# Optimization experiments

Measured on AMD Instinct MI355X. Metric: run time of the kernel, lower is better.

Reference implementation:

```python
import jax, jax.numpy as jnp
import numpy as np

C, S, Q, P, D = 5, 5, 75, 196, 384  # ways, shots, queries, patches, feat dim
K = 30  # topk in enhancePrototypes / featureWalk


def _bn(x, g, b, eps=1e-5):
    # BatchNorm1d in training mode: batch statistics (biased var)
    m = x.mean(axis=0)
    v = x.var(axis=0)
    return g * (x - m) * jax.lax.rsqrt(v + eps) + b


def _mlp(x, W1, b1, g1, be1, al, W2, b2, g2, be2):
    # fc1 -> bn1 -> PReLU -> (dropout=identity, eval) -> fc2 -> bn2
    h = _bn(x @ W1 + b1, g1, be1)
    h = jnp.where(h >= 0, h, al * h)
    h = h @ W2 + b2
    return _bn(h, g2, be2)


def _enhance_prototypes(cls_tok, patch, k=K, a=1.0):
    # cls_tok: (C,S,D), patch: (C,S,P,D)
    dist = jnp.linalg.norm(cls_tok[:, :, None, :] - patch, axis=3)  # (C,S,P)
    d0 = dist[:, 0, :]                       # (C,P) -- source uses [0] row
    other = d0.sum(axis=0)[None, :] - d0     # sum over other classes, shot 0
    sim = dist / (other[:, None, :] + 1e-6)  # (C,S,P)
    _, idx = jax.lax.top_k(sim, k)           # (C,S,k)
    sel = jnp.take_along_axis(patch, idx[..., None], axis=2)  # (C,S,k,D)
    return cls_tok * 2.0 + a * sel.mean(axis=2)


def _feature_walk(prototypes, q_patch, cls_tok, k=K, a=1.0):
    # prototypes: (C,D), q_patch: (Q,P,D), cls_tok: (Q,D)
    dot = jnp.einsum('cd,qpd->cqp', prototypes, q_patch)
    n_p = jnp.linalg.norm(prototypes, axis=1)      # (C,)
    n_q = jnp.linalg.norm(q_patch, axis=2)         # (Q,P)
    cos = dot / jnp.maximum(n_p[:, None, None] * n_q[None], 1e-8)
    w = jax.nn.softmax(cos, axis=2)                # (C,Q,P)
    vals, idx = jax.lax.top_k(w, k)                # (C,Q,k)
    gathered = q_patch[jnp.arange(Q)[None, :, None], idx]  # (C,Q,k,D)
    wsum = jnp.einsum('cqk,cqkd->cqd', vals, gathered)
    return cls_tok[None] * 2.0 + a * wsum          # (C,Q,D)


def setup_inputs() -> dict:
    key = jax.random.key(0)
    ks = jax.random.split(key, 12)
    r = lambda i, shape, s=1.0: jax.random.normal(ks[i], shape, dtype=jnp.float32) * s
    inp = {
        'support_set_vectors': r(0, (C * S, 1, D)),
        'query_set_vectors': r(1, (Q, 1, D)),
        'dalle_emb_support': r(2, (C * S, 1, D)),
        'emb_patch_support': r(3, (C * S, P, D)),
        'emb_patch_query': r(4, (Q, P, D)),
        'dalle_patch_embedding': r(5, (C * S, P, D)),
    }
    i = 6
    for pre in ('da', 'pa'):
        inp[pre + '_W1'] = r(i, (D, D), 0.05)
        inp[pre + '_b1'] = jnp.zeros((D,), jnp.float32)
        inp[pre + '_g1'] = jnp.ones((D,), jnp.float32)
        inp[pre + '_be1'] = jnp.zeros((D,), jnp.float32)
        inp[pre + '_al'] = jnp.float32(0.25)  # PReLU default init
        inp[pre + '_W2'] = r(i + 1, (D, D), 0.05)
        inp[pre + '_b2'] = jnp.zeros((D,), jnp.float32)
        inp[pre + '_g2'] = jnp.ones((D,), jnp.float32)
        inp[pre + '_be2'] = jnp.zeros((D,), jnp.float32)
        i += 2
    return inp


def reference(support_set_vectors, query_set_vectors, dalle_emb_support,
              emb_patch_support, emb_patch_query, dalle_patch_embedding,
              da_W1, da_b1, da_g1, da_be1, da_al, da_W2, da_b2, da_g2, da_be2,
              pa_W1, pa_b1, pa_g1, pa_be1, pa_al, pa_W2, pa_b2, pa_g2, pa_be2):
    da = (da_W1, da_b1, da_g1, da_be1, da_al, da_W2, da_b2, da_g2, da_be2)
    pa = (pa_W1, pa_b1, pa_g1, pa_be1, pa_al, pa_W2, pa_b2, pa_g2, pa_be2)

    sup = support_set_vectors.reshape(C, S, D)
    qcls = query_set_vectors.reshape(Q, D)

    dalle_sup = _mlp(dalle_emb_support.reshape(-1, D), *da).reshape(C, S, D)
    dalle_patch = _mlp(dalle_patch_embedding.reshape(-1, D), *da).reshape(-1, P, D)

    eps_ = emb_patch_support + _mlp(emb_patch_support.reshape(-1, D), *pa).reshape(-1, P, D)
    epq = emb_patch_query + _mlp(emb_patch_query.reshape(-1, D), *pa).reshape(-1, P, D)
    dalle_patch = dalle_patch + _mlp(dalle_patch.reshape(-1, D), *pa).reshape(-1, P, D)

    ep = jnp.concatenate([
        _enhance_prototypes(sup, eps_.reshape(C, S, P, D)),
        _enhance_prototypes(dalle_sup, dalle_patch.reshape(C, S, P, D)),
    ], axis=1).mean(axis=1)  # (C,D)

    cls_with_weighted_sums = _feature_walk(ep, epq, qcls)  # (C,Q,D)
    return ep, cls_with_weighted_sums
```

## Files before the change

### kernel.cpp

```cpp
#include <hip/hip_runtime.h>


#define CC 5
#define SS 5
#define QQ 75
#define PP 196
#define DD 384
#define KK 30
#define QP (QQ * PP)

typedef short bf16x8 __attribute__((ext_vector_type(8)));
typedef float f32x4  __attribute__((ext_vector_type(4)));
typedef unsigned short us16x4 __attribute__((ext_vector_type(4)));
typedef unsigned short us16x8 __attribute__((ext_vector_type(8)));
typedef unsigned short u16;

struct SegDesc { int b0, b1; float invM; };

__device__ __forceinline__ u16 f2bf(float f) {
    unsigned u = __float_as_uint(f);
    unsigned r = (u + 0x7fffu + ((u >> 16) & 1u)) >> 16;
    return (u16)r;
}
__device__ __forceinline__ float bf2f(u16 h) {
    return __uint_as_float((unsigned)h << 16);
}

__device__ __forceinline__ void lds_load16(const u16* g, u16* s) {
    __builtin_amdgcn_global_load_lds(
        (const __attribute__((address_space(1))) unsigned int*)g,
        (__attribute__((address_space(3))) unsigned int*)s, 16, 0, 0);
}

__device__ __forceinline__ bool grid_decode(int mb, int& mblk, int& nb) {
    int bid = blockIdx.x;
    int g = bid / 24, t24 = bid - g * 24;
    nb = t24 >> 3;
    mblk = g * 8 + (t24 & 7);
    return mblk < mb;
}

__device__ __forceinline__ void do_mfma64(const u16* Asb, const u16* Bsb,
                                          int wr, int wc, int l, f32x4 (&acc)[2][4]) {
#pragma unroll
    for (int ks = 0; ks < 2; ++ks) {
        bf16x8 af[2], bg[4];
#pragma unroll
        for (int i = 0; i < 2; ++i) {
            int rm = wr * 32 + i * 16 + (l & 15);
            af[i] = *(const bf16x8*)&Asb[rm * 64 + (((ks << 2) + (l >> 4)) ^ (rm & 7)) * 8];
        }
#pragma unroll
        for (int j = 0; j < 4; ++j) {
            int rn = wc * 64 + j * 16 + (l & 15);
            bg[j] = *(const bf16x8*)&Bsb[rn * 64 + (((ks << 2) + (l >> 4)) ^ (rn & 7)) * 8];
        }
#pragma unroll
        for (int i = 0; i < 2; ++i)
#pragma unroll
            for (int j = 0; j < 4; ++j)
                acc[i][j] = __builtin_amdgcn_mfma_f32_16x16x32_bf16(af[i], bg[j], acc[i][j], 0, 0, 0);
    }
}

__global__ void prep_w4(const float* __restrict__ W0, const float* __restrict__ W1,
                        const float* __restrict__ W2, const float* __restrict__ W3,
                        u16* __restrict__ Wt) {
    int idx = blockIdx.x * 256 + threadIdx.x;
    int m = idx / (DD * DD);
    int rem = idx - m * (DD * DD);
    int n = rem / DD, k = rem - n * DD;
    const float* W = (m == 0) ? W0 : (m == 1) ? W1 : (m == 2) ? W2 : W3;
    Wt[idx] = f2bf(W[k * DD + n]);
}

__global__ __launch_bounds__(256) void gemmF(const float* __restrict__ s0p,
                                             const float* __restrict__ s1p,
                                             const float* __restrict__ s2p,
                                             int rb0, int rb1, int M0, int M1, int M2,
                                             const u16* __restrict__ Bt,
                                             u16* __restrict__ H,
                                             float* __restrict__ partial, int mb) {
    __shared__ __align__(16) u16 As[2][4096];
    __shared__ __align__(16) u16 Bs[2][8192];
    __shared__ float sred[2][2][64][2];
    int mblk, nb;
    if (!grid_decode(mb, mblk, nb)) return;
    const int m0 = mblk * 64, n0 = nb * 128;
    const int tid = threadIdx.x;
    const int w = tid >> 6, l = tid & 63;
    const int wr = w >> 1, wc = w & 1;
    const int lr8 = l >> 3, kpB = l & 7;
    const int arow = tid >> 2, kp0 = (tid & 3) * 2;
    const int aslot0 = kp0 ^ (arow & 7);

    const int seg = (m0 >= rb0) + (m0 >= rb1);
    const float* src = seg == 0 ? s0p : seg == 1 ? s1p : s2p;
    const int segbase = seg == 0 ? 0 : seg == 1 ? rb0 : rb1;
    const int Mseg = seg == 0 ? M0 : seg == 1 ? M1 : M2;
    const int rloc = m0 - segbase + arow;

    f32x4 acc[2][4];
#pragma unroll
    for (int i = 0; i < 2; ++i)
#pragma unroll
        for (int j = 0; j < 4; ++j) acc[i][j] = f32x4{0.f, 0.f, 0.f, 0.f};

    f32x4 ra[4];
    auto issueA = [&](int kta) {
#pragma unroll
        for (int i = 0; i < 4; ++i) ra[i] = f32x4{0.f, 0.f, 0.f, 0.f};
        if (rloc < Mseg) {
            const f32x4* sp = (const f32x4*)(src + (size_t)rloc * DD + kta * 64 + kp0 * 8);
#pragma unroll
            for (int i = 0; i < 4; ++i) ra[i] = sp[i];
        }
    };
    auto stageB = [&](int kta, int b) {
#pragma unroll
        for (int i = 0; i < 4; ++i) {
            int row = i * 32 + w * 8 + lr8;
            lds_load16(Bt + (size_t)(n0 + row) * DD + kta * 64 + (kpB ^ (row & 7)) * 8,
                       &Bs[b][i * 2048 + w * 512]);
        }
    };
    auto writeA = [&](int b) {
        us16x8 o0, o1;
        o0[0] = f2bf(ra[0].x); o0[1] = f2bf(ra[0].y); o0[2] = f2bf(ra[0].z); o0[3] = f2bf(ra[0].w);
        o0[4] = f2bf(ra[1].x); o0[5] = f2bf(ra[1].y); o0[6] = f2bf(ra[1].z); o0[7] = f2bf(ra[1].w);
        o1[0] = f2bf(ra[2].x); o1[1] = f2bf(ra[2].y); o1[2] = f2bf(ra[2].z); o1[3] = f2bf(ra[2].w);
        o1[4] = f2bf(ra[3].x); o1[5] = f2bf(ra[3].y); o1[6] = f2bf(ra[3].z); o1[7] = f2bf(ra[3].w);
        *(us16x8*)&As[b][arow * 64 + aslot0 * 8] = o0;
        *(us16x8*)&As[b][arow * 64 + (aslot0 ^ 1) * 8] = o1;
    };

    issueA(0);
    stageB(0, 0);
    writeA(0);
    __syncthreads();
    int cur = 0;
    for (int kt = 0; kt < 5; ++kt) {
        int nxt = cur ^ 1;
        issueA(kt + 1);
        stageB(kt + 1, nxt);
        do_mfma64(&As[cur][0], &Bs[cur][0], wr, wc, l, acc);
        writeA(nxt);
        __syncthreads();
        cur = nxt;
    }
    do_mfma64(&As[cur][0], &Bs[cur][0], wr, wc, l, acc);

#pragma unroll
    for (int i = 0; i < 2; ++i) {
        int rw0 = m0 + wr * 32 + i * 16 + ((l >> 4) << 2);
#pragma unroll
        for (int j = 0; j < 4; ++j) {
            int col = n0 + wc * 64 + j * 16 + (l & 15);
#pragma unroll
            for (int r = 0; r < 4; ++r)
                H[(size_t)(rw0 + r) * DD + col] = f2bf(acc[i][j][r]);
        }
    }
    float ls[4], ls2[4];
#pragma unroll
    for (int j = 0; j < 4; ++j) { ls[j] = 0.f; ls2[j] = 0.f; }
#pragma unroll
    for (int i = 0; i < 2; ++i)
#pragma unroll
        for (int j = 0; j < 4; ++j)
#pragma unroll
            for (int r = 0; r < 4; ++r) {
                float v = acc[i][j][r];
                ls[j] += v; ls2[j] += v * v;
            }
#pragma unroll
    for (int j = 0; j < 4; ++j) {
        ls[j]  += __shfl_xor(ls[j], 16);  ls[j]  += __shfl_xor(ls[j], 32);
        ls2[j] += __shfl_xor(ls2[j], 16); ls2[j] += __shfl_xor(ls2[j], 32);
    }
    if ((l >> 4) == 0) {
#pragma unroll
        for (int j = 0; j < 4; ++j) {
            sred[wr][wc][j * 16 + (l & 15)][0] = ls[j];
            sred[wr][wc][j * 16 + (l & 15)][1] = ls2[j];
        }
    }
    __syncthreads();
    if (tid < 128) {
        int wcx = tid >> 6, c64 = tid & 63;
        float sa = sred[0][wcx][c64][0] + sred[1][wcx][c64][0];
        float sb = sred[0][wcx][c64][1] + sred[1][wcx][c64][1];
        size_t pi = ((size_t)mblk * DD + n0 + tid) * 2;
        partial[pi] = sa; partial[pi + 1] = sb;
    }
}

__global__ __launch_bounds__(256) void gemmA(const u16* __restrict__ Hs,
                                             int rb0, int rb1, int M0, int M1, int M2,
                                             const u16* __restrict__ Bt,
                                             const float* __restrict__ alp,
                                             const float* __restrict__ mstats,
                                             u16* __restrict__ H2,
                                             float* __restrict__ partial, int mb) {
    __shared__ __align__(16) u16 As[2][4096];
    __shared__ __align__(16) u16 Bs[2][8192];
    __shared__ float sred[2][2][64][2];
    __shared__ __align__(16) float msL[768];
    int mblk, nb;
    if (!grid_decode(mb, mblk, nb)) return;
    const int m0 = mblk * 64, n0 = nb * 128;
    const int tid = threadIdx.x;
    const int w = tid >> 6, l = tid & 63;
    const int wr = w >> 1, wc = w & 1;
    const int lr8 = l >> 3, kpB = l & 7;
    const int arow = tid >> 2, kp0 = (tid & 3) * 2;
    const int aslot0 = kp0 ^ (arow & 7);

    const int seg = (m0 >= rb0) + (m0 >= rb1);
    const int segbase = seg == 0 ? 0 : seg == 1 ? rb0 : rb1;
    const int Mseg = seg == 0 ? M0 : seg == 1 ? M1 : M2;
    const int rloc = m0 - segbase + arow;
    const float al = *alp;

    if (tid < 192) ((f32x4*)msL)[tid] = ((const f32x4*)(mstats + seg * 768))[tid];

    f32x4 acc[2][4];
#pragma unroll
    for (int i = 0; i < 2; ++i)
#pragma unroll
        for (int j = 0; j < 4; ++j) acc[i][j] = f32x4{0.f, 0.f, 0.f, 0.f};

    us16x8 rh[2];
    auto issueA = [&](int kta) {
        rh[0] = us16x8{0, 0, 0, 0, 0, 0, 0, 0};
        rh[1] = us16x8{0, 0, 0, 0, 0, 0, 0, 0};
        if (rloc < Mseg) {
            const us16x8* sp = (const us16x8*)(Hs + (size_t)(m0 + arow) * DD + kta * 64 + kp0 * 8);
            rh[0] = sp[0]; rh[1] = sp[1];
        }
    };
    auto stageB = [&](int kta, int b) {
#pragma unroll
        for (int i = 0; i < 4; ++i) {
            int row = i * 32 + w * 8 + lr8;
            lds_load16(Bt + (size_t)(n0 + row) * DD + kta * 64 + (kpB ^ (row & 7)) * 8,
                       &Bs[b][i * 2048 + w * 512]);
        }
    };
    auto writeA = [&](int kta, int b) {
        int cb = kta * 64 + kp0 * 8;
        us16x8 o0 = {0, 0, 0, 0, 0, 0, 0, 0}, o1 = {0, 0, 0, 0, 0, 0, 0, 0};
        if (rloc < Mseg) {
            f32x4 sc0 = *(const f32x4*)&msL[cb];
            f32x4 sc1 = *(const f32x4*)&msL[cb + 4];
            f32x4 sc2 = *(const f32x4*)&msL[cb + 8];
            f32x4 sc3 = *(const f32x4*)&msL[cb + 12];
            f32x4 sh0 = *(const f32x4*)&msL[384 + cb];
            f32x4 sh1 = *(const f32x4*)&msL[384 + cb + 4];
            f32x4 sh2 = *(const f32x4*)&msL[384 + cb + 8];
            f32x4 sh3 = *(const f32x4*)&msL[384 + cb + 12];
            float v;
            v = bf2f(rh[0][0]) * sc0.x + sh0.x; v = v >= 0.f ? v : al * v; o0[0] = f2bf(v);
            v = bf2f(rh[0][1]) * sc0.y + sh0.y; v = v >= 0.f ? v : al * v; o0[1] = f2bf(v);
            v = bf2f(rh[0][2]) * sc0.z + sh0.z; v = v >= 0.f ? v : al * v; o0[2] = f2bf(v);
            v = bf2f(rh[0][3]) * sc0.w + sh0.w; v = v >= 0.f ? v : al * v; o0[3] = f2bf(v);
            v = bf2f(rh[0][4]) * sc1.x + sh1.x; v = v >= 0.f ? v : al * v; o0[4] = f2bf(v);
            v = bf2f(rh[0][5]) * sc1.y + sh1.y; v = v >= 0.f ? v : al * v; o0[5] = f2bf(v);
            v = bf2f(rh[0][6]) * sc1.z + sh1.z; v = v >= 0.f ? v : al * v; o0[6] = f2bf(v);
            v = bf2f(rh[0][7]) * sc1.w + sh1.w; v = v >= 0.f ? v : al * v; o0[7] = f2bf(v);
            v = bf2f(rh[1][0]) * sc2.x + sh2.x; v = v >= 0.f ? v : al * v; o1[0] = f2bf(v);
            v = bf2f(rh[1][1]) * sc2.y + sh2.y; v = v >= 0.f ? v : al * v; o1[1] = f2bf(v);
            v = bf2f(rh[1][2]) * sc2.z + sh2.z; v = v >= 0.f ? v : al * v; o1[2] = f2bf(v);
            v = bf2f(rh[1][3]) * sc2.w + sh2.w; v = v >= 0.f ? v : al * v; o1[3] = f2bf(v);
            v = bf2f(rh[1][4]) * sc3.x + sh3.x; v = v >= 0.f ? v : al * v; o1[4] = f2bf(v);
            v = bf2f(rh[1][5]) * sc3.y + sh3.y; v = v >= 0.f ? v : al * v; o1[5] = f2bf(v);
            v = bf2f(rh[1][6]) * sc3.z + sh3.z; v = v >= 0.f ? v : al * v; o1[6] = f2bf(v);
            v = bf2f(rh[1][7]) * sc3.w + sh3.w; v = v >= 0.f ? v : al * v; o1[7] = f2bf(v);
        }
        *(us16x8*)&As[b][arow * 64 + aslot0 * 8] = o0;
        *(us16x8*)&As[b][arow * 64 + (aslot0 ^ 1) * 8] = o1;
    };

    issueA(0);
    stageB(0, 0);
    __syncthreads();
    writeA(0, 0);
    __syncthreads();
    int cur = 0;
    for (int kt = 0; kt < 5; ++kt) {
        int nxt = cur ^ 1;
        issueA(kt + 1);
        stageB(kt + 1, nxt);
        do_mfma64(&As[cur][0], &Bs[cur][0], wr, wc, l, acc);
        writeA(kt + 1, nxt);
        __syncthreads();
        cur = nxt;
    }
    do_mfma64(&As[cur][0], &Bs[cur][0], wr, wc, l, acc);

#pragma unroll
    for (int i = 0; i < 2; ++i) {
        int rw0 = m0 + wr * 32 + i * 16 + ((l >> 4) << 2);
#pragma unroll
        for (int j = 0; j < 4; ++j) {
            int col = n0 + wc * 64 + j * 16 + (l & 15);
#pragma unroll
            for (int r = 0; r < 4; ++r)
                H2[(size_t)(rw0 + r) * DD + col] = f2bf(acc[i][j][r]);
        }
    }
    float ls[4], ls2[4];
#pragma unroll
    for (int j = 0; j < 4; ++j) { ls[j] = 0.f; ls2[j] = 0.f; }
#pragma unroll
    for (int i = 0; i < 2; ++i)
#pragma unroll
        for (int j = 0; j < 4; ++j)
#pragma unroll
            for (int r = 0; r < 4; ++r) {
                float v = acc[i][j][r];
                ls[j] += v; ls2[j] += v * v;
            }
#pragma unroll
    for (int j = 0; j < 4; ++j) {
        ls[j]  += __shfl_xor(ls[j], 16);  ls[j]  += __shfl_xor(ls[j], 32);
        ls2[j] += __shfl_xor(ls2[j], 16); ls2[j] += __shfl_xor(ls2[j], 32);
    }
    if ((l >> 4) == 0) {
#pragma unroll
        for (int j = 0; j < 4; ++j) {
            sred[wr][wc][j * 16 + (l & 15)][0] = ls[j];
            sred[wr][wc][j * 16 + (l & 15)][1] = ls2[j];
        }
    }
    __syncthreads();
    if (tid < 128) {
        int wcx = tid >> 6, c64 = tid & 63;
        float sa = sred[0][wcx][c64][0] + sred[1][wcx][c64][0];
        float sb = sred[0][wcx][c64][1] + sred[1][wcx][c64][1];
        size_t pi = ((size_t)mblk * DD + n0 + tid) * 2;
        partial[pi] = sa; partial[pi + 1] = sb;
    }
}

__global__ void colfin(const float* __restrict__ partial, SegDesc s0, SegDesc s1,
                       SegDesc s2, const float* __restrict__ g,
                       const float* __restrict__ be, float* __restrict__ mstats) {
    int seg = blockIdx.x / 12, cg = blockIdx.x - seg * 12;
    SegDesc sd = (seg == 0) ? s0 : (seg == 1) ? s1 : s2;
    int tid = threadIdx.x;
    int col = cg * 32 + (tid & 31);
    int part = tid >> 5;
    float sa = 0.f, sb = 0.f;
    for (int b = sd.b0 + part; b < sd.b1; b += 8) {
        size_t pi = ((size_t)b * DD + col) * 2;
        sa += partial[pi]; sb += partial[pi + 1];
    }
    __shared__ float red[256][2];
    red[tid][0] = sa; red[tid][1] = sb;
    __syncthreads();
    for (int st = 128; st >= 32; st >>= 1) {
        if (tid < st) { red[tid][0] += red[tid + st][0]; red[tid][1] += red[tid + st][1]; }
        __syncthreads();
    }
    if (tid < 32) {
        float m = red[tid][0] * sd.invM;
        float var = fmaxf(red[tid][1] * sd.invM - m * m, 0.f);
        float iv = rsqrtf(var + 1e-5f);
        int c = cg * 32 + tid;
        float sc = iv * g[c];
        mstats[seg * 768 + c] = sc;
        mstats[seg * 768 + 384 + c] = be[c] - m * sc;
    }
}

__global__ void mlp_out_k(const u16* __restrict__ H, const float* __restrict__ mstats,
                          const float* __restrict__ res0, float* __restrict__ out0,
                          const float* __restrict__ res1, float* __restrict__ out1,
                          const float* __restrict__ res2, float* __restrict__ out2,
                          int rb0, int rb1, int M0, int M1, int M2) {
    int idx4 = blockIdx.x * 256 + threadIdx.x;
    int row = idx4 / 96, cq = idx4 - row * 96, col = cq * 4;
    int seg = (row >= rb0) + (row >= rb1);
    int vr = row - (seg == 1 ? rb0 : seg == 2 ? rb1 : 0);
    int M = seg == 0 ? M0 : seg == 1 ? M1 : M2;
    const float* res = seg == 0 ? res0 : seg == 1 ? res1 : res2;
    float* outf = seg == 0 ? out0 : seg == 1 ? out1 : out2;
    f32x4 v = {0.f, 0.f, 0.f, 0.f};
    if (vr < M) {
        us16x4 h = ((const us16x4*)H)[idx4];
        const float* ms = mstats + seg * 768;
        f32x4 sc = *(const f32x4*)(ms + col);
        f32x4 sh = *(const f32x4*)(ms + 384 + col);
        v.x = bf2f(h.x) * sc.x + sh.x;
        v.y = bf2f(h.y) * sc.y + sh.y;
        v.z = bf2f(h.z) * sc.z + sh.z;
        v.w = bf2f(h.w) * sc.w + sh.w;
        if (res) {
            f32x4 r = ((const f32x4*)res)[(size_t)vr * 96 + cq];
            v.x += r.x; v.y += r.y; v.z += r.z; v.w += r.w;
        }
    }
    ((f32x4*)outf)[(size_t)vr * 96 + cq] = v;
}

__global__ void dist_k(const float* __restrict__ epsP, const float* __restrict__ dpfP,
                       const float* __restrict__ supC, const float* __restrict__ dsupC,
                       float* __restrict__ dist) {
    int id = blockIdx.x;
    int b = id / (CC * SS * PP);
    int r = id - b * (CC * SS * PP);
    int cs = r / PP;
    const float* patch = b ? dpfP : epsP;
    const float* cls = b ? dsupC : supC;
    int l = threadIdx.x;
    const float* pr = patch + (size_t)r * DD;
    const float* cr = cls + (size_t)cs * DD;
    float s = 0.f;
    for (int d = l; d < DD; d += 64) { float df = cr[d] - pr[d]; s += df * df; }
#pragma unroll
    for (int off = 32; off > 0; off >>= 1) s += __shfl_xor(s, off);
    if (l == 0) dist[id] = sqrtf(s);
}

__global__ void enh_k(const float* __restrict__ dist, const float* __restrict__ epsP,
                      const float* __restrict__ dpfP, const float* __restrict__ supC,
                      const float* __restrict__ dsupC, float* __restrict__ enh) {
    int id = blockIdx.x;
    int b = id / 25, cs = id - b * 25, c = cs / SS;
    int t = threadIdx.x;
    __shared__ float sim[PP];
    __shared__ int sidx[KK];
    const float* db = dist + b * (CC * SS * PP);
    if (t < PP) {
        float osum = 0.f;
        for (int cc = 0; cc < CC; ++cc) osum += db[cc * SS * PP + t];
        float other = osum - db[c * SS * PP + t];
        sim[t] = db[cs * PP + t] / (other + 1e-6f);
    }
    __syncthreads();
    if (t < PP) {
        float mine = sim[t];
        int cnt = 0;
        for (int p = 0; p < PP; ++p) {
            float v = sim[p];
            cnt += (v > mine) || (v == mine && p < t);
        }
        if (cnt < KK) sidx[cnt] = t;
    }
    __syncthreads();
    const float* patch = b ? dpfP : epsP;
    const float* cls = b ? dsupC : supC;
    float sum = 0.f;
#pragma unroll
    for (int j = 0; j < KK; ++j) sum += patch[((size_t)cs * PP + sidx[j]) * DD + t];
    enh[(size_t)id * DD + t] = 2.f * cls[(size_t)cs * DD + t] + sum * (1.f / 30.f);
}

__global__ void ep_k(const float* __restrict__ enh, float* __restrict__ outEp,
                     float* __restrict__ npb) {
    int t = threadIdx.x;
    __shared__ float red[DD];
    for (int c = 0; c < CC; ++c) {
        float v = 0.f;
        for (int b = 0; b < 2; ++b)
            for (int s = 0; s < SS; ++s)
                v += enh[((b * 25) + (c * SS + s)) * DD + t];
        v *= 0.1f;
        outEp[c * DD + t] = v;
        red[t] = v * v;
        __syncthreads();
        if (t < 64) {
            float s = 0.f;
            for (int i = t; i < DD; i += 64) s += red[i];
#pragma unroll
            for (int off = 32; off > 0; off >>= 1) s += __shfl_xor(s, off);
            if (t == 0) npb[c] = sqrtf(s);
        }
        __syncthreads();
    }
}

__global__ void cos_k(const float* __restrict__ epq, const float* __restrict__ ep,
                      const float* __restrict__ npb, float* __restrict__ eB) {
    __shared__ __align__(16) float epl[CC * DD];
    __shared__ float npl[CC];
    int t = threadIdx.x;
    for (int i = t; i < CC * DD; i += 256) epl[i] = ep[i];
    if (t < CC) npl[t] = npb[t];
    __syncthreads();
    int wid = t >> 6, l = t & 63;
    int row = blockIdx.x * 4 + wid;
    const float4* rp = (const float4*)(epq + (size_t)row * DD);
    const float4* e4 = (const float4*)epl;
    float nq = 0.f, dot[CC];
#pragma unroll
    for (int c = 0; c < CC; ++c) dot[c] = 0.f;
    for (int c4 = l; c4 < DD / 4; c4 += 64) {
        float4 x = rp[c4];
        nq += x.x * x.x + x.y * x.y + x.z * x.z + x.w * x.w;
#pragma unroll
        for (int c = 0; c < CC; ++c) {
            float4 e = e4[c * (DD / 4) + c4];
            dot[c] += e.x * x.x + e.y * x.y + e.z * x.z + e.w * x.w;
        }
    }
#pragma unroll
    for (int off = 32; off > 0; off >>= 1) {
        nq += __shfl_xor(nq, off);
#pragma unroll
        for (int c = 0; c < CC; ++c) dot[c] += __shfl_xor(dot[c], off);
    }
    if (l == 0) {
        float sq = sqrtf(nq);
#pragma unroll
        for (int c = 0; c < CC; ++c)
            eB[c * QP + row] = expf(dot[c] / fmaxf(npl[c] * sq, 1e-8f) - 1.f);
    }
}

__global__ void walk2_k(const float* __restrict__ eB, const float* __restrict__ epq,
                        const float* __restrict__ qcls, float* __restrict__ outp) {
    int bid = blockIdx.x;
    int c = bid / QQ, q = bid - c * QQ;
    int t = threadIdx.x;
    __shared__ float wv[PP];
    __shared__ float red[256];
    __shared__ float sval[KK];
    __shared__ int sidx[KK];
    float e = 0.f;
    if (t < PP) { e = eB[c * QP + q * PP + t]; wv[t] = e; }
    red[t] = e;
    __syncthreads();
    for (int st = 128; st > 0; st >>= 1) { if (t < st) red[t] += red[t + st]; __syncthreads(); }
    float inv = 1.f / red[0];
    if (t < PP) {
        int cnt = 0;
        for (int p = 0; p < PP; ++p) {
            float v = wv[p];
            cnt += (v > e) || (v == e && p < t);
        }
        if (cnt < KK) { sval[cnt] = e * inv; sidx[cnt] = t; }
    }
    __syncthreads();
    const float* eb = epq + (size_t)q * PP * DD;
    for (int d = t; d < DD; d += 256) {
        float a = 0.f;
#pragma unroll
        for (int j = 0; j < KK; ++j) a += sval[j] * eb[(size_t)sidx[j] * DD + d];
        outp[(size_t)bid * DD + d] = 2.f * qcls[q * DD + d] + a;
    }
}

extern "C" void kernel_launch(void* const* d_in, const int* in_sizes, int n_in,
                              void* d_out, int out_size, void* d_ws, size_t ws_size,
                              hipStream_t stream) {
    const float* sup   = (const float*)d_in[0];
    const float* qcls  = (const float*)d_in[1];
    const float* dsupI = (const float*)d_in[2];
    const float* epsI  = (const float*)d_in[3];
    const float* epqI  = (const float*)d_in[4];
    const float* dpI   = (const float*)d_in[5];
    const float* daW1 = (const float*)d_in[6],  *daG1 = (const float*)d_in[8],
               * daBe1 = (const float*)d_in[9], *daAl = (const float*)d_in[10];
    const float* daW2 = (const float*)d_in[11], *daG2 = (const float*)d_in[13],
               * daBe2 = (const float*)d_in[14];
    const float* paW1 = (const float*)d_in[15], *paG1 = (const float*)d_in[17],
               * paBe1 = (const float*)d_in[18], *paAl = (const float*)d_in[19];
    const float* paW2 = (const float*)d_in[20], *paG2 = (const float*)d_in[22],
               * paBe2 = (const float*)d_in[23];

    char* ws = (char*)d_ws;
    size_t off = 0;
    auto alloc = [&](size_t b) -> void* {
        void* p = ws + off;
        off = (off + b + 255) & ~(size_t)255;
        return p;
    };
    const int MP_S = 128;
    const int M_P = 4900,  MP_P = 4992;
    const int M_Q = 14700, MP_Qa = 14848;
    const int ROWS_A  = MP_S + MP_P;
    const int ROWS_BC = MP_P + MP_Qa + MP_P;
    const int RB0 = MP_P, RB1 = MP_P + MP_Qa;

    u16*   wtAll = (u16*)alloc((size_t)4 * DD * DD * 2);
    u16*   wtDa1 = wtAll;
    u16*   wtDa2 = wtAll + DD * DD;
    u16*   wtPa1 = wtAll + 2 * DD * DD;
    u16*   wtPa2 = wtAll + 3 * DD * DD;
    u16*   hbuf  = (u16*)alloc((size_t)ROWS_BC * DD * 2);
    u16*   a2buf = (u16*)alloc((size_t)ROWS_BC * DD * 2);
    float* partial = (float*)alloc((size_t)(ROWS_BC / 64) * DD * 2 * 4);
    float* mstats  = (float*)alloc(3 * 768 * 4);
    float* dalleSup = (float*)alloc((size_t)MP_S * DD * 4);
    float* dp0   = (float*)alloc((size_t)MP_P * DD * 4);
    float* epsB  = (float*)alloc((size_t)MP_P * DD * 4);
    float* epqB  = (float*)alloc((size_t)MP_Qa * DD * 4);
    float* dpfB  = (float*)alloc((size_t)MP_P * DD * 4);
    float* distB = (float*)alloc((size_t)2 * CC * SS * PP * 4);
    float* enhB  = (float*)alloc((size_t)50 * DD * 4);
    float* npB   = (float*)alloc(64);
    float* eB    = (float*)alloc((size_t)CC * QP * 4);

    prep_w4<<<4 * 576, 256, 0, stream>>>(daW1, daW2, paW1, paW2, wtAll);

    {
        int mb = ROWS_A / 64;
        int nblk = ((mb + 7) / 8) * 24;
        SegDesc s0{0, 2, 1.f / 25.f}, s1{2, mb, 1.f / 4900.f}, sx{0, 0, 1.f};
        int g96 = (ROWS_A * 96) / 256;
        gemmF<<<nblk, 256, 0, stream>>>(dsupI, dpI, nullptr, MP_S, ROWS_A,
                                        25, M_P, 0, wtDa1, hbuf, partial, mb);
        colfin<<<24, 256, 0, stream>>>(partial, s0, s1, sx, daG1, daBe1, mstats);
        gemmA<<<nblk, 256, 0, stream>>>(hbuf, MP_S, ROWS_A, 25, M_P, 0,
                                        wtDa2, daAl, mstats, a2buf, partial, mb);
        colfin<<<24, 256, 0, stream>>>(partial, s0, s1, sx, daG2, daBe2, mstats);
        mlp_out_k<<<g96, 256, 0, stream>>>(a2buf, mstats,
                                           nullptr, dalleSup,
                                           nullptr, dp0,
                                           nullptr, nullptr,
                                           MP_S, ROWS_A, 25, M_P, 0);
    }

    {
        int mb = ROWS_BC / 64;
        int nblk = ((mb + 7) / 8) * 24;
        SegDesc s0{0, RB0 / 64, 1.f / 4900.f},
                s1{RB0 / 64, RB1 / 64, 1.f / 14700.f},
                s2{RB1 / 64, mb, 1.f / 4900.f};
        int g96 = (ROWS_BC * 96) / 256;
        gemmF<<<nblk, 256, 0, stream>>>(epsI, epqI, dp0, RB0, RB1,
                                        M_P, M_Q, M_P, wtPa1, hbuf, partial, mb);
        colfin<<<36, 256, 0, stream>>>(partial, s0, s1, s2, paG1, paBe1, mstats);
        gemmA<<<nblk, 256, 0, stream>>>(hbuf, RB0, RB1, M_P, M_Q, M_P,
                                        wtPa2, paAl, mstats, a2buf, partial, mb);
        colfin<<<36, 256, 0, stream>>>(partial, s0, s1, s2, paG2, paBe2, mstats);
        mlp_out_k<<<g96, 256, 0, stream>>>(a2buf, mstats,
                                           epsI, epsB,
                                           epqI, epqB,
                                           dp0, dpfB,
                                           RB0, RB1, M_P, M_Q, M_P);
    }

    dist_k<<<2 * CC * SS * PP, 64, 0, stream>>>(epsB, dpfB, sup, dalleSup, distB);
    enh_k<<<2 * CC * SS, 384, 0, stream>>>(distB, epsB, dpfB, sup, dalleSup, enhB);

    float* outEp = (float*)d_out;
    float* outW = (float*)d_out + CC * DD;
    ep_k<<<1, 384, 0, stream>>>(enhB, outEp, npB);

    cos_k<<<QP / 4, 256, 0, stream>>>(epqB, outEp, npB, eB);
    walk2_k<<<CC * QQ, 256, 0, stream>>>(eB, epqB, qcls, outW);
}
```

Measured before the change: 177.3 us.

## Fuse tail stages into one cooperative persistent kernel with grid syncs

Replaces the last colfin, mlp_out, dist, enhance, ep, cos and walk kernels with a single cooperative kernel of 375 blocks that runs each stage in turn, separated by grid.sync(). The aim is to remove the launch overhead and inter-kernel gaps of seven small launches. In exchange, the large elementwise and cosine stages now run on only 375 blocks using grid-stride loops, and each grid barrier has its own cost. Several stages also leave most blocks idle.

```diff
diff --git a/kernel.cpp b/kernel.cpp
--- a/kernel.cpp
+++ b/kernel.cpp
@@ -1,4 +1,7 @@
 #include <hip/hip_runtime.h>
+#include <hip/hip_cooperative_groups.h>
+
+namespace cg = cooperative_groups;
 
 
 #define CC 5
@@ -346,10 +349,10 @@
 __global__ void colfin(const float* __restrict__ partial, SegDesc s0, SegDesc s1,
                        SegDesc s2, const float* __restrict__ g,
                        const float* __restrict__ be, float* __restrict__ mstats) {
-    int seg = blockIdx.x / 12, cg = blockIdx.x - seg * 12;
+    int seg = blockIdx.x / 12, cg_ = blockIdx.x - seg * 12;
     SegDesc sd = (seg == 0) ? s0 : (seg == 1) ? s1 : s2;
     int tid = threadIdx.x;
-    int col = cg * 32 + (tid & 31);
+    int col = cg_ * 32 + (tid & 31);
     int part = tid >> 5;
     float sa = 0.f, sb = 0.f;
     for (int b = sd.b0 + part; b < sd.b1; b += 8) {
@@ -367,7 +370,7 @@
         float m = red[tid][0] * sd.invM;
         float var = fmaxf(red[tid][1] * sd.invM - m * m, 0.f);
         float iv = rsqrtf(var + 1e-5f);
-        int c = cg * 32 + tid;
+        int c = cg_ * 32 + tid;
         float sc = iv * g[c];
         mstats[seg * 768 + c] = sc;
         mstats[seg * 768 + 384 + c] = be[c] - m * sc;
@@ -404,151 +407,216 @@
     ((f32x4*)outf)[(size_t)vr * 96 + cq] = v;
 }
 
-__global__ void dist_k(const float* __restrict__ epsP, const float* __restrict__ dpfP,
-                       const float* __restrict__ supC, const float* __restrict__ dsupC,
-                       float* __restrict__ dist) {
-    int id = blockIdx.x;
-    int b = id / (CC * SS * PP);
-    int r = id - b * (CC * SS * PP);
-    int cs = r / PP;
-    const float* patch = b ? dpfP : epsP;
-    const float* cls = b ? dsupC : supC;
-    int l = threadIdx.x;
-    const float* pr = patch + (size_t)r * DD;
-    const float* cr = cls + (size_t)cs * DD;
-    float s = 0.f;
-    for (int d = l; d < DD; d += 64) { float df = cr[d] - pr[d]; s += df * df; }
-#pragma unroll
-    for (int off = 32; off > 0; off >>= 1) s += __shfl_xor(s, off);
-    if (l == 0) dist[id] = sqrtf(s);
-}
-
-__global__ void enh_k(const float* __restrict__ dist, const float* __restrict__ epsP,
-                      const float* __restrict__ dpfP, const float* __restrict__ supC,
-                      const float* __restrict__ dsupC, float* __restrict__ enh) {
-    int id = blockIdx.x;
-    int b = id / 25, cs = id - b * 25, c = cs / SS;
-    int t = threadIdx.x;
+struct TailArgs {
+    const float* partial; SegDesc s0, s1, s2;
+    const float* g2; const float* be2; float* mstats;
+    const u16* H2;
+    const float* res0; float* out0;
+    const float* res1; float* out1;
+    const float* res2; float* out2;
+    int rb0, rb1, M0, M1, M2;
+    const float* supC; const float* dsupC;
+    float* dist; float* enh;
+    float* outEp; float* npb;
+    const float* qcls; float* eB; float* outW;
+};
+
+__global__ __launch_bounds__(256) void tail_k(TailArgs a) {
+    cg::grid_group grid = cg::this_grid();
+    const int bid = blockIdx.x;
+    const int tid = threadIdx.x;
+    const int wid = tid >> 6, l = tid & 63;
+    __shared__ float red2[256][2];
+    __shared__ float red1[256];
     __shared__ float sim[PP];
-    __shared__ int sidx[KK];
-    const float* db = dist + b * (CC * SS * PP);
-    if (t < PP) {
-        float osum = 0.f;
-        for (int cc = 0; cc < CC; ++cc) osum += db[cc * SS * PP + t];
-        float other = osum - db[c * SS * PP + t];
-        sim[t] = db[cs * PP + t] / (other + 1e-6f);
-    }
-    __syncthreads();
-    if (t < PP) {
-        float mine = sim[t];
-        int cnt = 0;
-        for (int p = 0; p < PP; ++p) {
-            float v = sim[p];
-            cnt += (v > mine) || (v == mine && p < t);
-        }
-        if (cnt < KK) sidx[cnt] = t;
-    }
-    __syncthreads();
-    const float* patch = b ? dpfP : epsP;
-    const float* cls = b ? dsupC : supC;
-    float sum = 0.f;
-#pragma unroll
-    for (int j = 0; j < KK; ++j) sum += patch[((size_t)cs * PP + sidx[j]) * DD + t];
-    enh[(size_t)id * DD + t] = 2.f * cls[(size_t)cs * DD + t] + sum * (1.f / 30.f);
-}
-
-__global__ void ep_k(const float* __restrict__ enh, float* __restrict__ outEp,
-                     float* __restrict__ npb) {
-    int t = threadIdx.x;
-    __shared__ float red[DD];
-    for (int c = 0; c < CC; ++c) {
-        float v = 0.f;
-        for (int b = 0; b < 2; ++b)
-            for (int s = 0; s < SS; ++s)
-                v += enh[((b * 25) + (c * SS + s)) * DD + t];
-        v *= 0.1f;
-        outEp[c * DD + t] = v;
-        red[t] = v * v;
-        __syncthreads();
-        if (t < 64) {
-            float s = 0.f;
-            for (int i = t; i < DD; i += 64) s += red[i];
-#pragma unroll
-            for (int off = 32; off > 0; off >>= 1) s += __shfl_xor(s, off);
-            if (t == 0) npb[c] = sqrtf(s);
-        }
-        __syncthreads();
-    }
-}
-
-__global__ void cos_k(const float* __restrict__ epq, const float* __restrict__ ep,
-                      const float* __restrict__ npb, float* __restrict__ eB) {
+    __shared__ float wv[PP];
+    __shared__ float sval[KK];
+    __shared__ int   sidx[KK];
     __shared__ __align__(16) float epl[CC * DD];
     __shared__ float npl[CC];
-    int t = threadIdx.x;
-    for (int i = t; i < CC * DD; i += 256) epl[i] = ep[i];
-    if (t < CC) npl[t] = npb[t];
+
+    if (bid < 36) {
+        int seg = bid / 12, cgp = bid - seg * 12;
+        SegDesc sd = (seg == 0) ? a.s0 : (seg == 1) ? a.s1 : a.s2;
+        int col = cgp * 32 + (tid & 31);
+        int part = tid >> 5;
+        float sa = 0.f, sb = 0.f;
+        for (int b = sd.b0 + part; b < sd.b1; b += 8) {
+            size_t pi = ((size_t)b * DD + col) * 2;
+            sa += a.partial[pi]; sb += a.partial[pi + 1];
+        }
+        red2[tid][0] = sa; red2[tid][1] = sb;
+        __syncthreads();
+        for (int st = 128; st >= 32; st >>= 1) {
+            if (tid < st) { red2[tid][0] += red2[tid + st][0]; red2[tid][1] += red2[tid + st][1]; }
+            __syncthreads();
+        }
+        if (tid < 32) {
+            float m = red2[tid][0] * sd.invM;
+            float var = fmaxf(red2[tid][1] * sd.invM - m * m, 0.f);
+            float iv = rsqrtf(var + 1e-5f);
+            int c = cgp * 32 + tid;
+            float sc = iv * a.g2[c];
+            a.mstats[seg * 768 + c] = sc;
+            a.mstats[seg * 768 + 384 + c] = a.be2[c] - m * sc;
+        }
+    }
+    grid.sync();
+
+    for (int chunk = bid; chunk < 9312; chunk += 375) {
+        int idx4 = chunk * 256 + tid;
+        int row = idx4 / 96, cq = idx4 - row * 96, col = cq * 4;
+        int seg = (row >= a.rb0) + (row >= a.rb1);
+        int vr = row - (seg == 1 ? a.rb0 : seg == 2 ? a.rb1 : 0);
+        int M = seg == 0 ? a.M0 : seg == 1 ? a.M1 : a.M2;
+        const float* res = seg == 0 ? a.res0 : seg == 1 ? a.res1 : a.res2;
+        float* outf = seg == 0 ? a.out0 : seg == 1 ? a.out1 : a.out2;
+        f32x4 v = {0.f, 0.f, 0.f, 0.f};
+        if (vr < M) {
+            us16x4 h = ((const us16x4*)a.H2)[idx4];
+            const float* ms = a.mstats + seg * 768;
+            f32x4 sc = *(const f32x4*)(ms + col);
+            f32x4 sh = *(const f32x4*)(ms + 384 + col);
+            v.x = bf2f(h.x) * sc.x + sh.x;
+            v.y = bf2f(h.y) * sc.y + sh.y;
+            v.z = bf2f(h.z) * sc.z + sh.z;
+            v.w = bf2f(h.w) * sc.w + sh.w;
+            f32x4 r = ((const f32x4*)res)[(size_t)vr * 96 + cq];
+            v.x += r.x; v.y += r.y; v.z += r.z; v.w += r.w;
+        }
+        ((f32x4*)outf)[(size_t)vr * 96 + cq] = v;
+    }
+    grid.sync();
+
+    for (int id = bid * 4 + wid; id < 2 * CC * SS * PP; id += 1500) {
+        int b = id / (CC * SS * PP);
+        int r = id - b * (CC * SS * PP);
+        int cs = r / PP;
+        const float* patch = b ? a.out2 : a.out0;
+        const float* cls = b ? a.dsupC : a.supC;
+        const float* pr = patch + (size_t)r * DD;
+        const float* cr = cls + (size_t)cs * DD;
+        float s = 0.f;
+        for (int d = l; d < DD; d += 64) { float df = cr[d] - pr[d]; s += df * df; }
+#pragma unroll
+        for (int off = 32; off > 0; off >>= 1) s += __shfl_xor(s, off);
+        if (l == 0) a.dist[id] = sqrtf(s);
+    }
+    grid.sync();
+
+    if (bid < 50) {
+        int b = bid / 25, cs = bid - b * 25, c = cs / SS;
+        const float* db = a.dist + b * (CC * SS * PP);
+        if (tid < PP) {
+            float osum = 0.f;
+            for (int cc = 0; cc < CC; ++cc) osum += db[cc * SS * PP + tid];
+            float other = osum - db[c * SS * PP + tid];
+            sim[tid] = db[cs * PP + tid] / (other + 1e-6f);
+        }
+        __syncthreads();
+        if (tid < PP) {
+            float mine = sim[tid];
+            int cnt = 0;
+            for (int p = 0; p < PP; ++p) {
+                float v = sim[p];
+                cnt += (v > mine) || (v == mine && p < tid);
+            }
+            if (cnt < KK) sidx[cnt] = tid;
+        }
+        __syncthreads();
+        const float* patch = b ? a.out2 : a.out0;
+        const float* cls = b ? a.dsupC : a.supC;
+        for (int d = tid; d < DD; d += 256) {
+            float sum = 0.f;
+#pragma unroll
+            for (int j = 0; j < KK; ++j) sum += patch[((size_t)cs * PP + sidx[j]) * DD + d];
+            a.enh[(size_t)bid * DD + d] = 2.f * cls[(size_t)cs * DD + d] + sum * (1.f / 30.f);
+        }
+    }
+    grid.sync();
+
+    if (bid < CC) {
+        int c = bid;
+        float ss = 0.f;
+        for (int t = tid; t < DD; t += 256) {
+            float v = 0.f;
+            for (int b = 0; b < 2; ++b)
+                for (int s = 0; s < SS; ++s)
+                    v += a.enh[((b * 25) + (c * SS + s)) * DD + t];
+            v *= 0.1f;
+            a.outEp[c * DD + t] = v;
+            ss += v * v;
+        }
+        red1[tid] = ss;
+        __syncthreads();
+        for (int st = 128; st > 0; st >>= 1) {
+            if (tid < st) red1[tid] += red1[tid + st];
+            __syncthreads();
+        }
+        if (tid == 0) a.npb[c] = sqrtf(red1[0]);
+    }
+    grid.sync();
+
+    for (int i = tid; i < CC * DD; i += 256) epl[i] = a.outEp[i];
+    if (tid < CC) npl[tid] = a.npb[tid];
     __syncthreads();
-    int wid = t >> 6, l = t & 63;
-    int row = blockIdx.x * 4 + wid;
-    const float4* rp = (const float4*)(epq + (size_t)row * DD);
-    const float4* e4 = (const float4*)epl;
-    float nq = 0.f, dot[CC];
-#pragma unroll
-    for (int c = 0; c < CC; ++c) dot[c] = 0.f;
-    for (int c4 = l; c4 < DD / 4; c4 += 64) {
-        float4 x = rp[c4];
-        nq += x.x * x.x + x.y * x.y + x.z * x.z + x.w * x.w;
-#pragma unroll
-        for (int c = 0; c < CC; ++c) {
-            float4 e = e4[c * (DD / 4) + c4];
-            dot[c] += e.x * x.x + e.y * x.y + e.z * x.z + e.w * x.w;
-        }
-    }
-#pragma unroll
-    for (int off = 32; off > 0; off >>= 1) {
-        nq += __shfl_xor(nq, off);
-#pragma unroll
-        for (int c = 0; c < CC; ++c) dot[c] += __shfl_xor(dot[c], off);
-    }
-    if (l == 0) {
-        float sq = sqrtf(nq);
-#pragma unroll
-        for (int c = 0; c < CC; ++c)
-            eB[c * QP + row] = expf(dot[c] / fmaxf(npl[c] * sq, 1e-8f) - 1.f);
-    }
-}
-
-__global__ void walk2_k(const float* __restrict__ eB, const float* __restrict__ epq,
-                        const float* __restrict__ qcls, float* __restrict__ outp) {
-    int bid = blockIdx.x;
-    int c = bid / QQ, q = bid - c * QQ;
-    int t = threadIdx.x;
-    __shared__ float wv[PP];
-    __shared__ float red[256];
-    __shared__ float sval[KK];
-    __shared__ int sidx[KK];
-    float e = 0.f;
-    if (t < PP) { e = eB[c * QP + q * PP + t]; wv[t] = e; }
-    red[t] = e;
-    __syncthreads();
-    for (int st = 128; st > 0; st >>= 1) { if (t < st) red[t] += red[t + st]; __syncthreads(); }
-    float inv = 1.f / red[0];
-    if (t < PP) {
-        int cnt = 0;
-        for (int p = 0; p < PP; ++p) {
-            float v = wv[p];
-            cnt += (v > e) || (v == e && p < t);
-        }
-        if (cnt < KK) { sval[cnt] = e * inv; sidx[cnt] = t; }
-    }
-    __syncthreads();
-    const float* eb = epq + (size_t)q * PP * DD;
-    for (int d = t; d < DD; d += 256) {
-        float a = 0.f;
-#pragma unroll
-        for (int j = 0; j < KK; ++j) a += sval[j] * eb[(size_t)sidx[j] * DD + d];
-        outp[(size_t)bid * DD + d] = 2.f * qcls[q * DD + d] + a;
+    for (int row = bid * 4 + wid; row < QP; row += 1500) {
+        const float4* rp = (const float4*)(a.out1 + (size_t)row * DD);
+        const float4* e4 = (const float4*)epl;
+        float nq = 0.f, dot[CC];
+#pragma unroll
+        for (int c = 0; c < CC; ++c) dot[c] = 0.f;
+        for (int c4 = l; c4 < DD / 4; c4 += 64) {
+            float4 x = rp[c4];
+            nq += x.x * x.x + x.y * x.y + x.z * x.z + x.w * x.w;
+#pragma unroll
+            for (int c = 0; c < CC; ++c) {
+                float4 e = e4[c * (DD / 4) + c4];
+                dot[c] += e.x * x.x + e.y * x.y + e.z * x.z + e.w * x.w;
+            }
+        }
+#pragma unroll
+        for (int off = 32; off > 0; off >>= 1) {
+            nq += __shfl_xor(nq, off);
+#pragma unroll
+            for (int c = 0; c < CC; ++c) dot[c] += __shfl_xor(dot[c], off);
+        }
+        if (l == 0) {
+            float sq = sqrtf(nq);
+#pragma unroll
+            for (int c = 0; c < CC; ++c)
+                a.eB[c * QP + row] = expf(dot[c] / fmaxf(npl[c] * sq, 1e-8f) - 1.f);
+        }
+    }
+    grid.sync();
+
+    {
+        int c = bid / QQ, q = bid - c * QQ;
+        float e = 0.f;
+        if (tid < PP) { e = a.eB[c * QP + q * PP + tid]; wv[tid] = e; }
+        red1[tid] = e;
+        __syncthreads();
+        for (int st = 128; st > 0; st >>= 1) {
+            if (tid < st) red1[tid] += red1[tid + st];
+            __syncthreads();
+        }
+        float inv = 1.f / red1[0];
+        if (tid < PP) {
+            int cnt = 0;
+            for (int p = 0; p < PP; ++p) {
+                float v = wv[p];
+                cnt += (v > e) || (v == e && p < tid);
+            }
+            if (cnt < KK) { sval[cnt] = e * inv; sidx[cnt] = tid; }
+        }
+        __syncthreads();
+        const float* eb = a.out1 + (size_t)q * PP * DD;
+        for (int d = tid; d < DD; d += 256) {
+            float acc = 0.f;
+#pragma unroll
+            for (int j = 0; j < KK; ++j) acc += sval[j] * eb[(size_t)sidx[j] * DD + d];
+            a.outW[(size_t)bid * DD + d] = 2.f * a.qcls[q * DD + d] + acc;
+        }
     }
 }
 
@@ -629,27 +697,28 @@
         SegDesc s0{0, RB0 / 64, 1.f / 4900.f},
                 s1{RB0 / 64, RB1 / 64, 1.f / 14700.f},
                 s2{RB1 / 64, mb, 1.f / 4900.f};
-        int g96 = (ROWS_BC * 96) / 256;
         gemmF<<<nblk, 256, 0, stream>>>(epsI, epqI, dp0, RB0, RB1,
                                         M_P, M_Q, M_P, wtPa1, hbuf, partial, mb);
         colfin<<<36, 256, 0, stream>>>(partial, s0, s1, s2, paG1, paBe1, mstats);
         gemmA<<<nblk, 256, 0, stream>>>(hbuf, RB0, RB1, M_P, M_Q, M_P,
                                         wtPa2, paAl, mstats, a2buf, partial, mb);
-        colfin<<<36, 256, 0, stream>>>(partial, s0, s1, s2, paG2, paBe2, mstats);
-        mlp_out_k<<<g96, 256, 0, stream>>>(a2buf, mstats,
-                                           epsI, epsB,
-                                           epqI, epqB,
-                                           dp0, dpfB,
-                                           RB0, RB1, M_P, M_Q, M_P);
-    }
-
-    dist_k<<<2 * CC * SS * PP, 64, 0, stream>>>(epsB, dpfB, sup, dalleSup, distB);
-    enh_k<<<2 * CC * SS, 384, 0, stream>>>(distB, epsB, dpfB, sup, dalleSup, enhB);
-
-    float* outEp = (float*)d_out;
-    float* outW = (float*)d_out + CC * DD;
-    ep_k<<<1, 384, 0, stream>>>(enhB, outEp, npB);
-
-    cos_k<<<QP / 4, 256, 0, stream>>>(epqB, outEp, npB, eB);
-    walk2_k<<<CC * QQ, 256, 0, stream>>>(eB, epqB, qcls, outW);
-}
+
+        float* outEp = (float*)d_out;
+        float* outW = (float*)d_out + CC * DD;
+        TailArgs ta;
+        ta.partial = partial; ta.s0 = s0; ta.s1 = s1; ta.s2 = s2;
+        ta.g2 = paG2; ta.be2 = paBe2; ta.mstats = mstats;
+        ta.H2 = a2buf;
+        ta.res0 = epsI; ta.out0 = epsB;
+        ta.res1 = epqI; ta.out1 = epqB;
+        ta.res2 = dp0;  ta.out2 = dpfB;
+        ta.rb0 = RB0; ta.rb1 = RB1; ta.M0 = M_P; ta.M1 = M_Q; ta.M2 = M_P;
+        ta.supC = sup; ta.dsupC = dalleSup;
+        ta.dist = distB; ta.enh = enhB;
+        ta.outEp = outEp; ta.npb = npB;
+        ta.qcls = qcls; ta.eB = eB; ta.outW = outW;
+        void* kargs[] = {&ta};
+        hipLaunchCooperativeKernel((const void*)tail_k, dim3(CC * QQ), dim3(256),
+                                   kargs, 0, stream);
+    }
+}
```

New measurement: 427.4 us. +141.0%, slower.
